# Performance work log

Hardware: AMD Instinct MI355X
Metric: run time of the kernel (lower is better)

## Reference

```python
import jax, jax.numpy as jnp
import numpy as np

B, L, D, N, H = 2, 2048, 1024, 16, 64  # batch, seq, d_model, heads, head_dim


def setup_inputs() -> dict:
    key = jax.random.key(0)
    k_x, k_qkv, k_proj = jax.random.split(key, 3)
    x = jax.random.normal(k_x, (B, L, D), dtype=jnp.float32)
    # RoPE table (L, H//2, 2) holding (cos, sin) per position/frequency
    inv_freq = 1.0 / (10000.0 ** (jnp.arange(H // 2, dtype=jnp.float32) / (H // 2)))
    ang = jnp.arange(L, dtype=jnp.float32)[:, None] * inv_freq[None, :]  # (L, H//2)
    rope = jnp.stack([jnp.cos(ang), jnp.sin(ang)], axis=-1)  # (L, H//2, 2)
    mask = jnp.tril(jnp.ones((L, L), dtype=bool))[None, None]  # (1,1,L,L) causal
    w_qkv = jax.random.normal(k_qkv, (D, 3 * D), dtype=jnp.float32) * 0.02
    w_proj = jax.random.normal(k_proj, (D, D), dtype=jnp.float32) * 0.02
    return {"x": x, "rope": rope, "mask": mask, "w_qkv": w_qkv, "w_proj": w_proj}


def _apply_rope(t, rope):
    # t: (B, L, N, H), rope: (L, H//2, 2)
    b, l, n, h = t.shape
    tp = t.reshape(b, l, n, h // 2, 2)
    cos = rope[None, :, None, :, 0]  # (1, L, 1, H//2)
    sin = rope[None, :, None, :, 1]
    t0, t1 = tp[..., 0], tp[..., 1]
    out = jnp.stack([t0 * cos - t1 * sin, t0 * sin + t1 * cos], axis=-1)
    return out.reshape(b, l, n, h)


def reference(x, rope, mask, w_qkv, w_proj):
    b, l, d = x.shape
    h = rope.shape[1] * 2
    n = d // h
    qkv = x @ w_qkv  # (b, l, 3d)
    q, k, v = jnp.split(qkv, 3, axis=2)
    q = _apply_rope(q.reshape(b, l, n, h), rope)
    k = _apply_rope(k.reshape(b, l, n, h), rope)
    v = v.reshape(b, l, n, h)
    scale = 1.0 / jnp.sqrt(jnp.asarray(h, dtype=x.dtype))
    scores = jnp.einsum('blnh,bmnh->bnlm', q, k) * scale  # (b, n, l, l)
    scores = jnp.where(mask, scores, jnp.finfo(scores.dtype).min)
    attn = jax.nn.softmax(scores, axis=-1)
    out = jnp.einsum('bnlm,bmnh->blnh', attn, v).reshape(b, l, d)
    return out @ w_proj
```

## Files before the change

### kernel.cpp

```cpp
#include <hip/hip_runtime.h>
#include <cmath>
#include <cstdint>


typedef __attribute__((ext_vector_type(8))) short bfrag8;
typedef __attribute__((ext_vector_type(4))) float f32x4;
typedef __attribute__((ext_vector_type(8))) unsigned short u16x8;

#define AS1 __attribute__((address_space(1)))
#define AS3 __attribute__((address_space(3)))

__device__ __forceinline__ unsigned short f2bf(float f) {
  uint32_t u = __builtin_bit_cast(uint32_t, f);
  u += 0x7fffu + ((u >> 16) & 1u);
  return (unsigned short)(u >> 16);
}
__device__ __forceinline__ float bf2f(unsigned short h) {
  return __builtin_bit_cast(float, (uint32_t)h << 16);
}
__device__ __forceinline__ int swz(int row, int bytecol) {
  return row * 128 + (bytecol ^ ((row & 7) << 4));
}

__global__ __launch_bounds__(256)
void f32_to_bf16_vec(const float* __restrict__ in, unsigned short* __restrict__ out, int n) {
  const int i = (blockIdx.x * 256 + threadIdx.x) * 4;
  if (i < n) {
    float4 v = *reinterpret_cast<const float4*>(in + i);
    ushort4 o;
    o.x = f2bf(v.x); o.y = f2bf(v.y); o.z = f2bf(v.z); o.w = f2bf(v.w);
    *reinterpret_cast<ushort4*>(out + i) = o;
  }
}

__global__ __launch_bounds__(256)
void transpose_f32_to_bf16(const float* __restrict__ w, unsigned short* __restrict__ wT,
                           int R, int C) {
  __shared__ float t[32][33];
  const int tx = threadIdx.x & 31, ty = threadIdx.x >> 5;
  const int c0 = blockIdx.x * 32, r0 = blockIdx.y * 32;
  #pragma unroll
  for (int s = 0; s < 32; s += 8)
    t[ty + s][tx] = w[(size_t)(r0 + ty + s) * C + c0 + tx];
  __syncthreads();
  #pragma unroll
  for (int s = 0; s < 32; s += 8)
    wT[(size_t)(c0 + ty + s) * R + r0 + tx] = f2bf(t[tx][ty + s]);
}

__global__ __launch_bounds__(256)
void gemm_bt_bf16(const unsigned short* __restrict__ A, const unsigned short* __restrict__ Bt,
                  void* __restrict__ Cout, int K, int ldC, int bf16_out) {
  __shared__ __align__(16) unsigned short As[128 * 64];
  __shared__ __align__(16) unsigned short Bs[128 * 64];

  const int tid  = threadIdx.x;
  const int brow = blockIdx.y * 128;
  const int bcol = blockIdx.x * 128;
  const int wid  = tid >> 6, lane = tid & 63;
  const int wr = (wid >> 1) * 64;
  const int wc = (wid & 1) * 64;
  const int lrow = lane & 15;
  const int lko  = (lane >> 4) * 8;
  const int srow  = tid >> 3;
  const int skoff = (tid & 7) * 8;

  f32x4 acc[4][4];
  #pragma unroll
  for (int m = 0; m < 4; ++m)
    #pragma unroll
    for (int n = 0; n < 4; ++n) acc[m][n] = (f32x4){0.f, 0.f, 0.f, 0.f};

  for (int k0 = 0; k0 < K; k0 += 64) {
    __syncthreads();
    #pragma unroll
    for (int i = 0; i < 4; ++i) {
      const int r = i * 32 + srow;
      __builtin_amdgcn_global_load_lds(
          (const AS1 void*)(A + (size_t)(brow + r) * K + k0 + skoff),
          (AS3 void*)(As + r * 64 + skoff), 16, 0, 0);
      __builtin_amdgcn_global_load_lds(
          (const AS1 void*)(Bt + (size_t)(bcol + r) * K + k0 + skoff),
          (AS3 void*)(Bs + r * 64 + skoff), 16, 0, 0);
    }
    __syncthreads();

    #pragma unroll
    for (int ks = 0; ks < 2; ++ks) {
      bfrag8 a[4], b[4];
      #pragma unroll
      for (int m = 0; m < 4; ++m)
        a[m] = *reinterpret_cast<const bfrag8*>(&As[(wr + m * 16 + lrow) * 64 + ks * 32 + lko]);
      #pragma unroll
      for (int n = 0; n < 4; ++n)
        b[n] = *reinterpret_cast<const bfrag8*>(&Bs[(wc + n * 16 + lrow) * 64 + ks * 32 + lko]);
      #pragma unroll
      for (int m = 0; m < 4; ++m)
        #pragma unroll
        for (int n = 0; n < 4; ++n)
          acc[m][n] = __builtin_amdgcn_mfma_f32_16x16x32_bf16(a[m], b[n], acc[m][n], 0, 0, 0);
    }
  }

  const int crow0 = brow + wr + (lane >> 4) * 4;
  const int ccol0 = bcol + wc + lrow;
  if (bf16_out) {
    unsigned short* C = (unsigned short*)Cout;
    #pragma unroll
    for (int m = 0; m < 4; ++m)
      #pragma unroll
      for (int n = 0; n < 4; ++n)
        #pragma unroll
        for (int r = 0; r < 4; ++r)
          C[(size_t)(crow0 + m * 16 + r) * ldC + ccol0 + n * 16] = f2bf(acc[m][n][r]);
  } else {
    float* C = (float*)Cout;
    #pragma unroll
    for (int m = 0; m < 4; ++m)
      #pragma unroll
      for (int n = 0; n < 4; ++n)
        #pragma unroll
        for (int r = 0; r < 4; ++r)
          C[(size_t)(crow0 + m * 16 + r) * ldC + ccol0 + n * 16] = acc[m][n][r];
  }
}

__global__ __launch_bounds__(256)
void rope_qk_kernel(const unsigned short* __restrict__ qk,
                    const float* __restrict__ rope,
                    unsigned short* __restrict__ Qr, unsigned short* __restrict__ Kr) {
  const int t = blockIdx.x * 256 + threadIdx.x;
  const int row = t >> 7;
  const int c8 = (t & 127) << 3;
  const int l = row & 2047;
  const float2* rp = (const float2*)rope + (size_t)l * 32 + ((c8 & 63) >> 1);

  u16x8 q = *reinterpret_cast<const u16x8*>(qk + (size_t)row * 2048 + c8);
  u16x8 k = *reinterpret_cast<const u16x8*>(qk + (size_t)row * 2048 + 1024 + c8);
  u16x8 qo, ko;
  #pragma unroll
  for (int p = 0; p < 4; ++p) {
    const float2 cs = rp[p];
    float q0 = bf2f(q[2 * p]), q1 = bf2f(q[2 * p + 1]);
    qo[2 * p]     = f2bf(q0 * cs.x - q1 * cs.y);
    qo[2 * p + 1] = f2bf(q0 * cs.y + q1 * cs.x);
    float k0 = bf2f(k[2 * p]), k1 = bf2f(k[2 * p + 1]);
    ko[2 * p]     = f2bf(k0 * cs.x - k1 * cs.y);
    ko[2 * p + 1] = f2bf(k0 * cs.y + k1 * cs.x);
  }
  *reinterpret_cast<u16x8*>(Qr + (size_t)row * 1024 + c8) = qo;
  *reinterpret_cast<u16x8*>(Kr + (size_t)row * 1024 + c8) = ko;
}

__global__ __launch_bounds__(256)
void v_transpose_kernel(const unsigned short* __restrict__ Vbuf,
                        unsigned short* __restrict__ Vt) {
  __shared__ unsigned short t[64][72];
  const int lt = blockIdx.x;
  const int bn = blockIdx.y;
  const int b = bn >> 4, n = bn & 15;
  const int r = threadIdx.x >> 2;
  const int cb = (threadIdx.x & 3) << 4;

  const unsigned short* src = Vbuf + (size_t)b * 2048 * 1024 + n * 64;
  #pragma unroll
  for (int c = 0; c < 2; ++c) {
    u16x8 v = *reinterpret_cast<const u16x8*>(src + (size_t)(lt * 64 + r) * 1024 + cb + c * 8);
    *reinterpret_cast<u16x8*>(&t[r][cb + c * 8]) = v;
  }
  __syncthreads();
  unsigned short* dst = Vt + ((size_t)bn * 64 + r) * 2048 + lt * 64;
  #pragma unroll
  for (int c = 0; c < 2; ++c) {
    u16x8 o;
    #pragma unroll
    for (int j = 0; j < 8; ++j) o[j] = t[cb + c * 8 + j][r];
    *reinterpret_cast<u16x8*>(dst + cb + c * 8) = o;
  }
}

__global__ __launch_bounds__(256)
void attn_mfma_kernel(const unsigned short* __restrict__ Qr,
                      const unsigned short* __restrict__ Kr,
                      const unsigned short* __restrict__ Vt,
                      unsigned short* __restrict__ out) {
  __shared__ __align__(16) unsigned short PQ_s[64 * 64];
  __shared__ __align__(16) unsigned short K_s [64 * 64];
  __shared__ __align__(16) unsigned short Vt_s[64 * 64];

  const int tid = threadIdx.x;
  const int wid = tid >> 6, lane = tid & 63;
  const int lrow = lane & 15;
  const int lko  = (lane >> 4) * 8;
  const int pairid = blockIdx.x >> 5;
  const int bn = blockIdx.x & 31;
  const int b = bn >> 4, n = bn & 15;

  const unsigned short* qb = Qr + (size_t)b * 2048 * 1024 + n * 64;
  const unsigned short* kb = Kr + (size_t)b * 2048 * 1024 + n * 64;
  const unsigned short* vb = Vt + (size_t)bn * 64 * 2048;
  unsigned short* ob = out + (size_t)b * 2048 * 1024 + n * 64;

  const int srow = lane >> 3;
  const int sgr  = (lane & 7) ^ srow;

  #pragma unroll 1
  for (int sel = 0; sel < 2; ++sel) {
    const int qt = sel ? pairid : 31 - pairid;

    __syncthreads();
    #pragma unroll
    for (int i = 0; i < 2; ++i) {
      const int row = i * 32 + wid * 8 + srow;
      __builtin_amdgcn_global_load_lds(
          (const AS1 void*)(qb + (size_t)(qt * 64 + row) * 1024 + sgr * 8),
          (AS3 void*)(PQ_s + (i * 32 + wid * 8) * 64 + lane * 8), 16, 0, 0);
    }
    __syncthreads();

    bfrag8 aq[2];
    #pragma unroll
    for (int ks = 0; ks < 2; ++ks)
      aq[ks] = *reinterpret_cast<const bfrag8*>(
          (const char*)PQ_s + swz(wid * 16 + lrow, (ks * 32 + lko) * 2));

    f32x4 oa[4];
    float m_r[4], l_r[4];
    #pragma unroll
    for (int r = 0; r < 4; ++r) { m_r[r] = -INFINITY; l_r[r] = 0.f; }
    #pragma unroll
    for (int nn = 0; nn < 4; ++nn) oa[nn] = (f32x4){0.f, 0.f, 0.f, 0.f};

    for (int kt = 0; kt <= qt; ++kt) {
      __syncthreads();
      #pragma unroll
      for (int i = 0; i < 2; ++i) {
        const int row = i * 32 + wid * 8 + srow;
        __builtin_amdgcn_global_load_lds(
            (const AS1 void*)(kb + (size_t)(kt * 64 + row) * 1024 + sgr * 8),
            (AS3 void*)(K_s + (i * 32 + wid * 8) * 64 + lane * 8), 16, 0, 0);
        __builtin_amdgcn_global_load_lds(
            (const AS1 void*)(vb + (size_t)row * 2048 + kt * 64 + sgr * 8),
            (AS3 void*)(Vt_s + (i * 32 + wid * 8) * 64 + lane * 8), 16, 0, 0);
      }
      __syncthreads();

      f32x4 s[4];
      #pragma unroll
      for (int nn = 0; nn < 4; ++nn) s[nn] = (f32x4){0.f, 0.f, 0.f, 0.f};
      __builtin_amdgcn_s_setprio(1);
      #pragma unroll
      for (int ks = 0; ks < 2; ++ks) {
        #pragma unroll
        for (int nn = 0; nn < 4; ++nn) {
          bfrag8 bk = *reinterpret_cast<const bfrag8*>(
              (const char*)K_s + swz(nn * 16 + lrow, (ks * 32 + lko) * 2));
          s[nn] = __builtin_amdgcn_mfma_f32_16x16x32_bf16(aq[ks], bk, s[nn], 0, 0, 0);
        }
      }
      __builtin_amdgcn_s_setprio(0);

      const bool diag = (kt == qt);
      #pragma unroll
      for (int r = 0; r < 4; ++r) {
        const int lrow_q = wid * 16 + (lane >> 4) * 4 + r;
        float mx = -INFINITY;
        #pragma unroll
        for (int nn = 0; nn < 4; ++nn) {
          float v = s[nn][r] * 0.125f;
          if (diag && (nn * 16 + lrow) > lrow_q) v = -INFINITY;
          s[nn][r] = v;
          mx = fmaxf(mx, v);
        }
        mx = fmaxf(mx, __shfl_xor(mx, 1));
        mx = fmaxf(mx, __shfl_xor(mx, 2));
        mx = fmaxf(mx, __shfl_xor(mx, 4));
        mx = fmaxf(mx, __shfl_xor(mx, 8));
        const float mnew = fmaxf(m_r[r], mx);
        const float alpha = __expf(m_r[r] - mnew);
        float rs = 0.f;
        unsigned short pb[4];
        #pragma unroll
        for (int nn = 0; nn < 4; ++nn) {
          const float p = __expf(s[nn][r] - mnew);
          pb[nn] = f2bf(p);
          rs += bf2f(pb[nn]);
        }
        rs += __shfl_xor(rs, 1);
        rs += __shfl_xor(rs, 2);
        rs += __shfl_xor(rs, 4);
        rs += __shfl_xor(rs, 8);
        l_r[r] = l_r[r] * alpha + rs;
        m_r[r] = mnew;
        #pragma unroll
        for (int nn = 0; nn < 4; ++nn) {
          oa[nn][r] *= alpha;
          *(unsigned short*)((char*)PQ_s + swz(lrow_q, (nn * 16 + lrow) * 2)) = pb[nn];
        }
      }

      __builtin_amdgcn_s_setprio(1);
      #pragma unroll
      for (int ks = 0; ks < 2; ++ks) {
        bfrag8 pa = *reinterpret_cast<const bfrag8*>(
            (const char*)PQ_s + swz(wid * 16 + lrow, (ks * 32 + lko) * 2));
        #pragma unroll
        for (int nn = 0; nn < 4; ++nn) {
          bfrag8 bv = *reinterpret_cast<const bfrag8*>(
              (const char*)Vt_s + swz(nn * 16 + lrow, (ks * 32 + lko) * 2));
          oa[nn] = __builtin_amdgcn_mfma_f32_16x16x32_bf16(pa, bv, oa[nn], 0, 0, 0);
        }
      }
      __builtin_amdgcn_s_setprio(0);
    }

    unsigned short* op = ob + (size_t)(qt * 64 + wid * 16 + (lane >> 4) * 4) * 1024;
    #pragma unroll
    for (int r = 0; r < 4; ++r) {
      const float inv = 1.f / l_r[r];
      #pragma unroll
      for (int nn = 0; nn < 4; ++nn)
        op[(size_t)r * 1024 + nn * 16 + lrow] = f2bf(oa[nn][r] * inv);
    }
  }
}

extern "C" void kernel_launch(void* const* d_in, const int* in_sizes, int n_in,
                              void* d_out, int out_size, void* d_ws, size_t ws_size,
                              hipStream_t stream) {
  (void)in_sizes; (void)n_in; (void)out_size; (void)ws_size;
  const float* x      = (const float*)d_in[0];
  const float* rope   = (const float*)d_in[1];
  const float* w_qkv  = (const float*)d_in[3];
  const float* w_proj = (const float*)d_in[4];
  float* out = (float*)d_out;

  const size_t MB = 1u << 20;
  char* ws = (char*)d_ws;
  unsigned short* x_bf   = (unsigned short*)(ws);
  unsigned short* Qrp    = (unsigned short*)(ws);
  unsigned short* wqkvT  = (unsigned short*)(ws + 8 * MB);
  unsigned short* Krp    = (unsigned short*)(ws + 8 * MB);
  unsigned short* qk     = (unsigned short*)(ws + 16 * MB);
  unsigned short* Vtp    = (unsigned short*)(ws + 16 * MB);
  unsigned short* Vbuf   = (unsigned short*)(ws + 32 * MB);
  unsigned short* wprojT = (unsigned short*)(ws + 32 * MB);
  unsigned short* attn   = (unsigned short*)(ws + 34 * MB);

  f32_to_bf16_vec<<<4096, 256, 0, stream>>>(x, x_bf, 4096 * 1024);
  transpose_f32_to_bf16<<<dim3(96, 32), 256, 0, stream>>>(w_qkv, wqkvT, 1024, 3072);

  gemm_bt_bf16<<<dim3(16, 32), 256, 0, stream>>>(x_bf, wqkvT, qk, 1024, 2048, 1);
  gemm_bt_bf16<<<dim3(8, 32), 256, 0, stream>>>(x_bf, wqkvT + (size_t)2048 * 1024, Vbuf,
                                                1024, 1024, 1);

  rope_qk_kernel<<<2048, 256, 0, stream>>>(qk, rope, Qrp, Krp);
  v_transpose_kernel<<<dim3(32, 32), 256, 0, stream>>>(Vbuf, Vtp);

  transpose_f32_to_bf16<<<dim3(32, 32), 256, 0, stream>>>(w_proj, wprojT, 1024, 1024);

  attn_mfma_kernel<<<512, 256, 0, stream>>>(Qrp, Krp, Vtp, attn);

  gemm_bt_bf16<<<dim3(8, 32), 256, 0, stream>>>(attn, wprojT, out, 1024, 1024, 0);
}
```

Baseline: 256.6 us.

## Double-buffer K/V tiles in attention, split blocks per q-tile, fuse QKV GEMM launches

```diff
diff --git a/kernel.cpp b/kernel.cpp
--- a/kernel.cpp
+++ b/kernel.cpp
@@ -50,7 +50,8 @@
 
 __global__ __launch_bounds__(256)
 void gemm_bt_bf16(const unsigned short* __restrict__ A, const unsigned short* __restrict__ Bt,
-                  void* __restrict__ Cout, int K, int ldC, int bf16_out) {
+                  void* __restrict__ C0, unsigned short* __restrict__ C1,
+                  int K, int ldC0, int ldC1, int splitcol, int bf16_out) {
   __shared__ __align__(16) unsigned short As[128 * 64];
   __shared__ __align__(16) unsigned short Bs[128 * 64];
 
@@ -104,24 +105,34 @@
 
   const int crow0 = brow + wr + (lane >> 4) * 4;
   const int ccol0 = bcol + wc + lrow;
-  if (bf16_out) {
-    unsigned short* C = (unsigned short*)Cout;
+  if (bcol >= splitcol) {
+    unsigned short* C = C1;
+    const int cc = ccol0 - splitcol;
     #pragma unroll
     for (int m = 0; m < 4; ++m)
       #pragma unroll
       for (int n = 0; n < 4; ++n)
         #pragma unroll
         for (int r = 0; r < 4; ++r)
-          C[(size_t)(crow0 + m * 16 + r) * ldC + ccol0 + n * 16] = f2bf(acc[m][n][r]);
-  } else {
-    float* C = (float*)Cout;
+          C[(size_t)(crow0 + m * 16 + r) * ldC1 + cc + n * 16] = f2bf(acc[m][n][r]);
+  } else if (bf16_out) {
+    unsigned short* C = (unsigned short*)C0;
     #pragma unroll
     for (int m = 0; m < 4; ++m)
       #pragma unroll
       for (int n = 0; n < 4; ++n)
         #pragma unroll
         for (int r = 0; r < 4; ++r)
-          C[(size_t)(crow0 + m * 16 + r) * ldC + ccol0 + n * 16] = acc[m][n][r];
+          C[(size_t)(crow0 + m * 16 + r) * ldC0 + ccol0 + n * 16] = f2bf(acc[m][n][r]);
+  } else {
+    float* C = (float*)C0;
+    #pragma unroll
+    for (int m = 0; m < 4; ++m)
+      #pragma unroll
+      for (int n = 0; n < 4; ++n)
+        #pragma unroll
+        for (int r = 0; r < 4; ++r)
+          C[(size_t)(crow0 + m * 16 + r) * ldC0 + ccol0 + n * 16] = acc[m][n][r];
   }
 }
 
@@ -142,8 +153,8 @@
   for (int p = 0; p < 4; ++p) {
     const float2 cs = rp[p];
     float q0 = bf2f(q[2 * p]), q1 = bf2f(q[2 * p + 1]);
-    qo[2 * p]     = f2bf(q0 * cs.x - q1 * cs.y);
-    qo[2 * p + 1] = f2bf(q0 * cs.y + q1 * cs.x);
+    qo[2 * p]     = f2bf((q0 * cs.x - q1 * cs.y) * 0.125f);
+    qo[2 * p + 1] = f2bf((q0 * cs.y + q1 * cs.x) * 0.125f);
     float k0 = bf2f(k[2 * p]), k1 = bf2f(k[2 * p + 1]);
     ko[2 * p]     = f2bf(k0 * cs.x - k1 * cs.y);
     ko[2 * p + 1] = f2bf(k0 * cs.y + k1 * cs.x);
@@ -185,15 +196,16 @@
                       const unsigned short* __restrict__ Vt,
                       unsigned short* __restrict__ out) {
   __shared__ __align__(16) unsigned short PQ_s[64 * 64];
-  __shared__ __align__(16) unsigned short K_s [64 * 64];
-  __shared__ __align__(16) unsigned short Vt_s[64 * 64];
+  __shared__ __align__(16) unsigned short K_s[2][64 * 64];
+  __shared__ __align__(16) unsigned short V_s[2][64 * 64];
 
   const int tid = threadIdx.x;
   const int wid = tid >> 6, lane = tid & 63;
   const int lrow = lane & 15;
   const int lko  = (lane >> 4) * 8;
-  const int pairid = blockIdx.x >> 5;
-  const int bn = blockIdx.x & 31;
+  const int i_blk = blockIdx.x;
+  const int qt = (i_blk < 512) ? (31 - (i_blk >> 5)) : ((i_blk - 512) >> 5);
+  const int bn = i_blk & 31;
   const int b = bn >> 4, n = bn & 15;
 
   const unsigned short* qb = Qr + (size_t)b * 2048 * 1024 + n * 64;
@@ -204,124 +216,128 @@
   const int srow = lane >> 3;
   const int sgr  = (lane & 7) ^ srow;
 
-  #pragma unroll 1
-  for (int sel = 0; sel < 2; ++sel) {
-    const int qt = sel ? pairid : 31 - pairid;
-
-    __syncthreads();
-    #pragma unroll
-    for (int i = 0; i < 2; ++i) {
-      const int row = i * 32 + wid * 8 + srow;
-      __builtin_amdgcn_global_load_lds(
-          (const AS1 void*)(qb + (size_t)(qt * 64 + row) * 1024 + sgr * 8),
-          (AS3 void*)(PQ_s + (i * 32 + wid * 8) * 64 + lane * 8), 16, 0, 0);
-    }
-    __syncthreads();
-
-    bfrag8 aq[2];
-    #pragma unroll
-    for (int ks = 0; ks < 2; ++ks)
-      aq[ks] = *reinterpret_cast<const bfrag8*>(
-          (const char*)PQ_s + swz(wid * 16 + lrow, (ks * 32 + lko) * 2));
-
-    f32x4 oa[4];
-    float m_r[4], l_r[4];
-    #pragma unroll
-    for (int r = 0; r < 4; ++r) { m_r[r] = -INFINITY; l_r[r] = 0.f; }
-    #pragma unroll
-    for (int nn = 0; nn < 4; ++nn) oa[nn] = (f32x4){0.f, 0.f, 0.f, 0.f};
-
-    for (int kt = 0; kt <= qt; ++kt) {
-      __syncthreads();
+  #pragma unroll
+  for (int i = 0; i < 2; ++i) {
+    const int row = i * 32 + wid * 8 + srow;
+    __builtin_amdgcn_global_load_lds(
+        (const AS1 void*)(qb + (size_t)(qt * 64 + row) * 1024 + sgr * 8),
+        (AS3 void*)(PQ_s + (i * 32 + wid * 8) * 64 + lane * 8), 16, 0, 0);
+    __builtin_amdgcn_global_load_lds(
+        (const AS1 void*)(kb + (size_t)(0 * 64 + row) * 1024 + sgr * 8),
+        (AS3 void*)(&K_s[0][(i * 32 + wid * 8) * 64 + lane * 8]), 16, 0, 0);
+    __builtin_amdgcn_global_load_lds(
+        (const AS1 void*)(vb + (size_t)row * 2048 + 0 * 64 + sgr * 8),
+        (AS3 void*)(&V_s[0][(i * 32 + wid * 8) * 64 + lane * 8]), 16, 0, 0);
+  }
+  __syncthreads();
+
+  bfrag8 aq[2];
+  #pragma unroll
+  for (int ks = 0; ks < 2; ++ks)
+    aq[ks] = *reinterpret_cast<const bfrag8*>(
+        (const char*)PQ_s + swz(wid * 16 + lrow, (ks * 32 + lko) * 2));
+
+  f32x4 oa[4];
+  float m_r[4], l_r[4];
+  #pragma unroll
+  for (int r = 0; r < 4; ++r) { m_r[r] = -INFINITY; l_r[r] = 0.f; }
+  #pragma unroll
+  for (int nn = 0; nn < 4; ++nn) oa[nn] = (f32x4){0.f, 0.f, 0.f, 0.f};
+
+  int cur = 0;
+  for (int kt = 0; kt <= qt; ++kt) {
+    if (kt < qt) {
       #pragma unroll
       for (int i = 0; i < 2; ++i) {
         const int row = i * 32 + wid * 8 + srow;
         __builtin_amdgcn_global_load_lds(
-            (const AS1 void*)(kb + (size_t)(kt * 64 + row) * 1024 + sgr * 8),
-            (AS3 void*)(K_s + (i * 32 + wid * 8) * 64 + lane * 8), 16, 0, 0);
+            (const AS1 void*)(kb + (size_t)((kt + 1) * 64 + row) * 1024 + sgr * 8),
+            (AS3 void*)(&K_s[cur ^ 1][(i * 32 + wid * 8) * 64 + lane * 8]), 16, 0, 0);
         __builtin_amdgcn_global_load_lds(
-            (const AS1 void*)(vb + (size_t)row * 2048 + kt * 64 + sgr * 8),
-            (AS3 void*)(Vt_s + (i * 32 + wid * 8) * 64 + lane * 8), 16, 0, 0);
-      }
-      __syncthreads();
-
-      f32x4 s[4];
-      #pragma unroll
-      for (int nn = 0; nn < 4; ++nn) s[nn] = (f32x4){0.f, 0.f, 0.f, 0.f};
-      __builtin_amdgcn_s_setprio(1);
-      #pragma unroll
-      for (int ks = 0; ks < 2; ++ks) {
-        #pragma unroll
-        for (int nn = 0; nn < 4; ++nn) {
-          bfrag8 bk = *reinterpret_cast<const bfrag8*>(
-              (const char*)K_s + swz(nn * 16 + lrow, (ks * 32 + lko) * 2));
-          s[nn] = __builtin_amdgcn_mfma_f32_16x16x32_bf16(aq[ks], bk, s[nn], 0, 0, 0);
-        }
-      }
-      __builtin_amdgcn_s_setprio(0);
-
-      const bool diag = (kt == qt);
-      #pragma unroll
-      for (int r = 0; r < 4; ++r) {
-        const int lrow_q = wid * 16 + (lane >> 4) * 4 + r;
-        float mx = -INFINITY;
-        #pragma unroll
-        for (int nn = 0; nn < 4; ++nn) {
-          float v = s[nn][r] * 0.125f;
-          if (diag && (nn * 16 + lrow) > lrow_q) v = -INFINITY;
-          s[nn][r] = v;
-          mx = fmaxf(mx, v);
-        }
-        mx = fmaxf(mx, __shfl_xor(mx, 1));
-        mx = fmaxf(mx, __shfl_xor(mx, 2));
-        mx = fmaxf(mx, __shfl_xor(mx, 4));
-        mx = fmaxf(mx, __shfl_xor(mx, 8));
-        const float mnew = fmaxf(m_r[r], mx);
-        const float alpha = __expf(m_r[r] - mnew);
-        float rs = 0.f;
-        unsigned short pb[4];
-        #pragma unroll
-        for (int nn = 0; nn < 4; ++nn) {
-          const float p = __expf(s[nn][r] - mnew);
-          pb[nn] = f2bf(p);
-          rs += bf2f(pb[nn]);
-        }
-        rs += __shfl_xor(rs, 1);
-        rs += __shfl_xor(rs, 2);
-        rs += __shfl_xor(rs, 4);
-        rs += __shfl_xor(rs, 8);
-        l_r[r] = l_r[r] * alpha + rs;
-        m_r[r] = mnew;
-        #pragma unroll
-        for (int nn = 0; nn < 4; ++nn) {
-          oa[nn][r] *= alpha;
-          *(unsigned short*)((char*)PQ_s + swz(lrow_q, (nn * 16 + lrow) * 2)) = pb[nn];
-        }
-      }
-
-      __builtin_amdgcn_s_setprio(1);
-      #pragma unroll
-      for (int ks = 0; ks < 2; ++ks) {
-        bfrag8 pa = *reinterpret_cast<const bfrag8*>(
-            (const char*)PQ_s + swz(wid * 16 + lrow, (ks * 32 + lko) * 2));
-        #pragma unroll
-        for (int nn = 0; nn < 4; ++nn) {
-          bfrag8 bv = *reinterpret_cast<const bfrag8*>(
-              (const char*)Vt_s + swz(nn * 16 + lrow, (ks * 32 + lko) * 2));
-          oa[nn] = __builtin_amdgcn_mfma_f32_16x16x32_bf16(pa, bv, oa[nn], 0, 0, 0);
-        }
-      }
-      __builtin_amdgcn_s_setprio(0);
-    }
-
-    unsigned short* op = ob + (size_t)(qt * 64 + wid * 16 + (lane >> 4) * 4) * 1024;
+            (const AS1 void*)(vb + (size_t)row * 2048 + (kt + 1) * 64 + sgr * 8),
+            (AS3 void*)(&V_s[cur ^ 1][(i * 32 + wid * 8) * 64 + lane * 8]), 16, 0, 0);
+      }
+    }
+    const char* Kb = (const char*)&K_s[cur][0];
+    const char* Vb = (const char*)&V_s[cur][0];
+
+    f32x4 s[4];
+    #pragma unroll
+    for (int nn = 0; nn < 4; ++nn) s[nn] = (f32x4){0.f, 0.f, 0.f, 0.f};
+    __builtin_amdgcn_s_setprio(1);
+    #pragma unroll
+    for (int ks = 0; ks < 2; ++ks) {
+      #pragma unroll
+      for (int nn = 0; nn < 4; ++nn) {
+        bfrag8 bk = *reinterpret_cast<const bfrag8*>(Kb + swz(nn * 16 + lrow, (ks * 32 + lko) * 2));
+        s[nn] = __builtin_amdgcn_mfma_f32_16x16x32_bf16(aq[ks], bk, s[nn], 0, 0, 0);
+      }
+    }
+    __builtin_amdgcn_s_setprio(0);
+
+    const bool diag = (kt == qt);
     #pragma unroll
     for (int r = 0; r < 4; ++r) {
-      const float inv = 1.f / l_r[r];
-      #pragma unroll
-      for (int nn = 0; nn < 4; ++nn)
-        op[(size_t)r * 1024 + nn * 16 + lrow] = f2bf(oa[nn][r] * inv);
-    }
+      const int lrow_q = wid * 16 + (lane >> 4) * 4 + r;
+      float mx = -INFINITY;
+      #pragma unroll
+      for (int nn = 0; nn < 4; ++nn) {
+        float v = s[nn][r];
+        if (diag && (nn * 16 + lrow) > lrow_q) v = -INFINITY;
+        s[nn][r] = v;
+        mx = fmaxf(mx, v);
+      }
+      mx = fmaxf(mx, __shfl_xor(mx, 1));
+      mx = fmaxf(mx, __shfl_xor(mx, 2));
+      mx = fmaxf(mx, __shfl_xor(mx, 4));
+      mx = fmaxf(mx, __shfl_xor(mx, 8));
+      const float mnew = fmaxf(m_r[r], mx);
+      const float alpha = __expf(m_r[r] - mnew);
+      float rs = 0.f;
+      unsigned short pb[4];
+      #pragma unroll
+      for (int nn = 0; nn < 4; ++nn) {
+        const float p = __expf(s[nn][r] - mnew);
+        pb[nn] = f2bf(p);
+        rs += bf2f(pb[nn]);
+      }
+      rs += __shfl_xor(rs, 1);
+      rs += __shfl_xor(rs, 2);
+      rs += __shfl_xor(rs, 4);
+      rs += __shfl_xor(rs, 8);
+      l_r[r] = l_r[r] * alpha + rs;
+      m_r[r] = mnew;
+      #pragma unroll
+      for (int nn = 0; nn < 4; ++nn) {
+        oa[nn][r] *= alpha;
+        *(unsigned short*)((char*)PQ_s + swz(lrow_q, (nn * 16 + lrow) * 2)) = pb[nn];
+      }
+    }
+
+    __builtin_amdgcn_s_setprio(1);
+    #pragma unroll
+    for (int ks = 0; ks < 2; ++ks) {
+      bfrag8 pa = *reinterpret_cast<const bfrag8*>(
+          (const char*)PQ_s + swz(wid * 16 + lrow, (ks * 32 + lko) * 2));
+      #pragma unroll
+      for (int nn = 0; nn < 4; ++nn) {
+        bfrag8 bv = *reinterpret_cast<const bfrag8*>(Vb + swz(nn * 16 + lrow, (ks * 32 + lko) * 2));
+        oa[nn] = __builtin_amdgcn_mfma_f32_16x16x32_bf16(pa, bv, oa[nn], 0, 0, 0);
+      }
+    }
+    __builtin_amdgcn_s_setprio(0);
+
+    __syncthreads();
+    cur ^= 1;
+  }
+
+  unsigned short* op = ob + (size_t)(qt * 64 + wid * 16 + (lane >> 4) * 4) * 1024;
+  #pragma unroll
+  for (int r = 0; r < 4; ++r) {
+    const float inv = 1.f / l_r[r];
+    #pragma unroll
+    for (int nn = 0; nn < 4; ++nn)
+      op[(size_t)r * 1024 + nn * 16 + lrow] = f2bf(oa[nn][r] * inv);
   }
 }
 
@@ -350,16 +366,16 @@
   f32_to_bf16_vec<<<4096, 256, 0, stream>>>(x, x_bf, 4096 * 1024);
   transpose_f32_to_bf16<<<dim3(96, 32), 256, 0, stream>>>(w_qkv, wqkvT, 1024, 3072);
 
-  gemm_bt_bf16<<<dim3(16, 32), 256, 0, stream>>>(x_bf, wqkvT, qk, 1024, 2048, 1);
-  gemm_bt_bf16<<<dim3(8, 32), 256, 0, stream>>>(x_bf, wqkvT + (size_t)2048 * 1024, Vbuf,
-                                                1024, 1024, 1);
+  gemm_bt_bf16<<<dim3(24, 32), 256, 0, stream>>>(x_bf, wqkvT, qk, Vbuf,
+                                                 1024, 2048, 1024, 2048, 1);
 
   rope_qk_kernel<<<2048, 256, 0, stream>>>(qk, rope, Qrp, Krp);
   v_transpose_kernel<<<dim3(32, 32), 256, 0, stream>>>(Vbuf, Vtp);
 
   transpose_f32_to_bf16<<<dim3(32, 32), 256, 0, stream>>>(w_proj, wprojT, 1024, 1024);
 
-  attn_mfma_kernel<<<512, 256, 0, stream>>>(Qrp, Krp, Vtp, attn);
-
-  gemm_bt_bf16<<<dim3(8, 32), 256, 0, stream>>>(attn, wprojT, out, 1024, 1024, 0);
-}
+  attn_mfma_kernel<<<1024, 256, 0, stream>>>(Qrp, Krp, Vtp, attn);
+
+  gemm_bt_bf16<<<dim3(8, 32), 256, 0, stream>>>(attn, wprojT, out, nullptr,
+                                                1024, 1024, 0, 1 << 30, 0);
+}
```

New measurement: 247.0 us. -3.7%, faster.
